# Optimization experiments

Measured on AMD Instinct MI355X. Metric: run time of the kernel, lower is better.

Reference implementation:

```python
import jax, jax.numpy as jnp
import numpy as np

D_MODEL = 1024
N_HEADS = 16
HEAD_DIM = D_MODEL // N_HEADS
D_FF = 4 * D_MODEL
EPS = 1e-5


def _layer_norm(h, g, b):
    m = jnp.mean(h, axis=-1, keepdims=True)
    v = jnp.mean(jnp.square(h - m), axis=-1, keepdims=True)
    return (h - m) * jax.lax.rsqrt(v + EPS) * g + b


def setup_inputs() -> dict:
    key = jax.random.key(0)
    ks = jax.random.split(key, 10)
    B, S, D = 4, 2048, D_MODEL
    scale = 0.02
    inp = {
        "x": jax.random.normal(ks[0], (B, S, D), dtype=jnp.float32),
        "Wq": scale * jax.random.normal(ks[1], (D, D), dtype=jnp.float32),
        "Wk": scale * jax.random.normal(ks[2], (D, D), dtype=jnp.float32),
        "Wv": scale * jax.random.normal(ks[3], (D, D), dtype=jnp.float32),
        "Wo": scale * jax.random.normal(ks[4], (D, D), dtype=jnp.float32),
        "ln1_g": jnp.ones((D,), dtype=jnp.float32),
        "ln1_b": jnp.zeros((D,), dtype=jnp.float32),
        "ln2_g": jnp.ones((D,), dtype=jnp.float32),
        "ln2_b": jnp.zeros((D,), dtype=jnp.float32),
        "W1": scale * jax.random.normal(ks[5], (D, D_FF), dtype=jnp.float32),
        "b1": jnp.zeros((D_FF,), dtype=jnp.float32),
        "W2": scale * jax.random.normal(ks[6], (D_FF, D), dtype=jnp.float32),
        "b2": jnp.zeros((D,), dtype=jnp.float32),
        "Wc": scale * jax.random.normal(ks[7], (D, 1), dtype=jnp.float32),
        "bc": jnp.zeros((1,), dtype=jnp.float32),
    }
    return inp


def reference(x, Wq, Wk, Wv, Wo, ln1_g, ln1_b, ln2_g, ln2_b, W1, b1, W2, b2, Wc, bc):
    B, S, D = x.shape
    H, hd = N_HEADS, HEAD_DIM
    # --- causal self-attention (pre-LN) ---
    h = _layer_norm(x, ln1_g, ln1_b)
    q = (h @ Wq).reshape(B, S, H, hd).transpose(0, 2, 1, 3)  # [B,H,S,hd]
    k = (h @ Wk).reshape(B, S, H, hd).transpose(0, 2, 1, 3)
    v = (h @ Wv).reshape(B, S, H, hd).transpose(0, 2, 1, 3)
    scores = jnp.einsum("bhqd,bhkd->bhqk", q, k) / jnp.sqrt(jnp.asarray(hd, x.dtype))
    causal = jnp.triu(jnp.ones((S, S), dtype=bool), k=1)
    scores = jnp.where(causal[None, None, :, :], -jnp.inf, scores)
    attn = jax.nn.softmax(scores, axis=-1)
    ctx = jnp.einsum("bhqk,bhkd->bhqd", attn, v).transpose(0, 2, 1, 3).reshape(B, S, D)
    x1 = x + ctx @ Wo
    # --- FFN (pre-LN, ReLU) ---
    h2 = _layer_norm(x1, ln2_g, ln2_b)
    ff = jax.nn.relu(h2 @ W1 + b1) @ W2 + b2
    x_out = x1 + ff
    # --- adaptive confidence gate: mean-pool seq -> Linear -> sigmoid -> batch mean ---
    pooled = jnp.mean(x_out, axis=1)  # [B,D]
    conf = jnp.mean(jax.nn.sigmoid(pooled @ Wc + bc), axis=0)  # [1]
    return x_out, conf
```

## Files before the change

kernel.cpp:

```cpp
#include <hip/hip_runtime.h>
#include <hip/hip_bf16.h>

typedef __hip_bfloat16 bf16;
typedef __attribute__((ext_vector_type(8))) short short8;
typedef __attribute__((ext_vector_type(4))) float f32x4;

#define D_MODELC 1024
#define D_FFC    4096
#define NHEADS   16
#define HDIM     64
#define SEQLEN   2048
#define BATCHN   4
#define MTOT     (BATCHN * SEQLEN)

__device__ __forceinline__ void async16(void* lds, const void* g) {
  __builtin_amdgcn_global_load_lds(
      (const __attribute__((address_space(1))) unsigned int*)g,
      (__attribute__((address_space(3))) unsigned int*)lds, 16, 0, 0);
}

__global__ __launch_bounds__(256) void transpose_bf16_k(
    const float* __restrict__ src, bf16* __restrict__ dst, int R, int C, float scale) {
  __shared__ float tile[32][33];
  int tx = threadIdx.x & 31, ty = threadIdx.x >> 5;
  int r0 = blockIdx.y * 32, c0 = blockIdx.x * 32;
#pragma unroll
  for (int i = 0; i < 4; i++) {
    int r = ty + i * 8;
    tile[r][tx] = src[(size_t)(r0 + r) * C + c0 + tx];
  }
  __syncthreads();
#pragma unroll
  for (int i = 0; i < 4; i++) {
    int c = ty + i * 8;
    dst[(size_t)(c0 + c) * R + r0 + tx] = __float2bfloat16(tile[tx][c] * scale);
  }
}

__global__ __launch_bounds__(256) void ln_bf16_k(
    const float* __restrict__ x, const float* __restrict__ g,
    const float* __restrict__ b, bf16* __restrict__ out) {
  int row = blockIdx.x;
  int t = threadIdx.x;
  f32x4 v = ((const f32x4*)(x + (size_t)row * D_MODELC))[t];
  float s = v[0] + v[1] + v[2] + v[3];
  float ss = v[0] * v[0] + v[1] * v[1] + v[2] * v[2] + v[3] * v[3];
#pragma unroll
  for (int m = 1; m < 64; m <<= 1) {
    s += __shfl_xor(s, m);
    ss += __shfl_xor(ss, m);
  }
  __shared__ float red[8];
  int w = t >> 6, l = t & 63;
  if (l == 0) { red[w] = s; red[4 + w] = ss; }
  __syncthreads();
  s = red[0] + red[1] + red[2] + red[3];
  ss = red[4] + red[5] + red[6] + red[7];
  float mean = s * (1.0f / D_MODELC);
  float var = ss * (1.0f / D_MODELC) - mean * mean;
  float rs = rsqrtf(var + 1e-5f);
  f32x4 gv = ((const f32x4*)g)[t];
  f32x4 bv = ((const f32x4*)b)[t];
  unsigned short u[4];
#pragma unroll
  for (int j = 0; j < 4; j++) {
    float o = (v[j] - mean) * rs * gv[j] + bv[j];
    u[j] = __bfloat16_as_ushort(__float2bfloat16(o));
  }
  unsigned int lo = (unsigned int)u[0] | ((unsigned int)u[1] << 16);
  unsigned int hi = (unsigned int)u[2] | ((unsigned int)u[3] << 16);
  ((uint2*)(out + (size_t)row * D_MODELC))[t] = make_uint2(lo, hi);
}

#define BM 128
#define BN 128
#define BKK 64

enum { EPI_QKV = 0, EPI_RESID = 1, EPI_BIAS_RELU = 2, EPI_BIAS_RESID = 3 };

template <int EPI>
__global__ __launch_bounds__(256) void gemm_nt(
    const bf16* __restrict__ A, const bf16* __restrict__ BT, int M, int N, int K,
    const float* __restrict__ bias, const float* __restrict__ resid,
    float* __restrict__ outF, bf16* __restrict__ outB) {
  __shared__ bf16 As[BM * BKK];
  __shared__ bf16 Bs[BN * BKK];
  const int t = threadIdx.x;
  const int l = t & 63;
  const int w = t >> 6;
  const int wm = w >> 1, wn = w & 1;

  int nwg = gridDim.x * gridDim.y;
  int bid = blockIdx.y * gridDim.x + blockIdx.x;
  if ((nwg & 7) == 0) {
    int q8 = nwg >> 3;
    bid = (bid & 7) * q8 + (bid >> 3);
  }
  const int bx = bid % gridDim.x, by = bid / gridDim.x;
  const int m0 = by * BM, n0 = bx * BN;
  const int lr = l & 15, lkg = l >> 4;

  f32x4 acc[4][4];
#pragma unroll
  for (int i = 0; i < 4; i++)
#pragma unroll
    for (int j = 0; j < 4; j++) acc[i][j] = (f32x4){0.f, 0.f, 0.f, 0.f};

  const char* Abase = (const char*)(A + (size_t)m0 * K);
  const char* Bbase = (const char*)(BT + (size_t)n0 * K);

  for (int k0 = 0; k0 < K; k0 += BKK) {
#pragma unroll
    for (int c = 0; c < 4; c++) {
      int off = (c * 256 + t) * 16;
      int r = off >> 7;
      int sg = ((off >> 4) & 7) ^ (r & 7);
      async16((char*)As + off, Abase + ((size_t)r * K + k0) * 2 + sg * 16);
      async16((char*)Bs + off, Bbase + ((size_t)r * K + k0) * 2 + sg * 16);
    }
    __syncthreads();
    short8 a[2][4], b[2][4];
#pragma unroll
    for (int kk = 0; kk < 2; kk++) {
#pragma unroll
      for (int mi = 0; mi < 4; mi++) {
        int row = wm * 64 + mi * 16 + lr;
        int sl = (kk * 4 + lkg) ^ (row & 7);
        a[kk][mi] = *(const short8*)((const char*)As + row * 128 + sl * 16);
      }
#pragma unroll
      for (int ni = 0; ni < 4; ni++) {
        int row = wn * 64 + ni * 16 + lr;
        int sl = (kk * 4 + lkg) ^ (row & 7);
        b[kk][ni] = *(const short8*)((const char*)Bs + row * 128 + sl * 16);
      }
    }
#pragma unroll
    for (int kk = 0; kk < 2; kk++)
#pragma unroll
      for (int mi = 0; mi < 4; mi++)
#pragma unroll
        for (int ni = 0; ni < 4; ni++)
          acc[mi][ni] = __builtin_amdgcn_mfma_f32_16x16x32_bf16(a[kk][mi], b[kk][ni], acc[mi][ni], 0, 0, 0);
    __syncthreads();
  }

#pragma unroll
  for (int mi = 0; mi < 4; mi++) {
#pragma unroll
    for (int ni = 0; ni < 4; ni++) {
#pragma unroll
      for (int j = 0; j < 4; j++) {
        int gm = m0 + wm * 64 + mi * 16 + ((l >> 4) * 4) + j;
        int gn = n0 + wn * 64 + ni * 16 + lr;
        float v = acc[mi][ni][j];
        if constexpr (EPI == EPI_QKV) {
          int sel = gn >> 10, d = gn & 1023;
          int b_ = gm >> 11, s_ = gm & 2047;
          int h2 = d >> 6, dd = d & 63;
          size_t bh = (size_t)b_ * NHEADS + h2;
          size_t dst;
          if (sel < 2) {
            dst = (size_t)sel * ((size_t)MTOT * D_MODELC) +
                  (bh * SEQLEN + s_) * HDIM + dd;
          } else {
            dst = 2 * ((size_t)MTOT * D_MODELC) +
                  (bh * HDIM + dd) * SEQLEN + s_;
          }
          outB[dst] = __float2bfloat16(v);
        } else if constexpr (EPI == EPI_RESID) {
          size_t idx = (size_t)gm * N + gn;
          outF[idx] = resid[idx] + v;
        } else if constexpr (EPI == EPI_BIAS_RELU) {
          float z = v + bias[gn];
          outB[(size_t)gm * N + gn] = __float2bfloat16(z > 0.f ? z : 0.f);
        } else {
          size_t idx = (size_t)gm * N + gn;
          outF[idx] = resid[idx] + v + bias[gn];
        }
      }
    }
  }
}

#define KVB 64
#define QB2 128
#define PSTR 76

__global__ __launch_bounds__(256) void attn_k(
    const bf16* __restrict__ qg, const bf16* __restrict__ kg,
    const bf16* __restrict__ vtg, bf16* __restrict__ ctx) {
  const int bid = blockIdx.x;
  const int qt = (SEQLEN / QB2 - 1) - (bid >> 6);
  const int bh = bid & 63;
  const int q0 = qt * QB2;
  const int t = threadIdx.x, w = t >> 6, l = t & 63;
  const int lr = l & 15, lkg = l >> 4, lk = lkg * 8;

  const bf16* Q  = qg  + (size_t)bh * SEQLEN * HDIM;
  const bf16* Kg = kg  + (size_t)bh * SEQLEN * HDIM;
  const bf16* Vt = vtg + (size_t)bh * HDIM * SEQLEN;

  __shared__ bf16 Ks[KVB * PSTR];
  __shared__ bf16 Vs[HDIM * PSTR];
  __shared__ bf16 Ps[4][32 * PSTR];

  short8 qf[2][2];
#pragma unroll
  for (int mi = 0; mi < 2; mi++)
#pragma unroll
    for (int kk = 0; kk < 2; kk++)
      qf[mi][kk] = *(const short8*)&Q[(size_t)(q0 + w * 32 + mi * 16 + lr) * HDIM + kk * 32 + lk];

  const short8 bones = {0x3F80, 0x3F80, 0x3F80, 0x3F80, 0x3F80, 0x3F80, 0x3F80, 0x3F80};

  f32x4 o[2][4];
  f32x4 ol[2];
#pragma unroll
  for (int mi = 0; mi < 2; mi++) {
    ol[mi] = (f32x4){0.f, 0.f, 0.f, 0.f};
#pragma unroll
    for (int nh = 0; nh < 4; nh++) o[mi][nh] = (f32x4){0.f, 0.f, 0.f, 0.f};
  }

  const int srow = t >> 3;
  const int scc  = (t & 7) * 8;

  const int ntiles = 2 * qt + 2;
  for (int tkv = 0; tkv < ntiles; tkv++) {
    const int kv0 = tkv * KVB;
#pragma unroll
    for (int r = 0; r < 2; r++) {
      int row = srow + r * 32;
      short8 kv = *(const short8*)&Kg[(size_t)(kv0 + row) * HDIM + scc];
      *(short8*)&Ks[row * PSTR + scc] = kv;
      short8 vv = *(const short8*)&Vt[(size_t)row * SEQLEN + kv0 + scc];
      *(short8*)&Vs[row * PSTR + scc] = vv;
    }
    __syncthreads();

    const bool active = (kv0 <= q0 + w * 32 + 31);
    if (active) {
      short8 kf[4][2];
#pragma unroll
      for (int ni = 0; ni < 4; ni++)
#pragma unroll
        for (int kk = 0; kk < 2; kk++)
          kf[ni][kk] = *(const short8*)&Ks[(ni * 16 + lr) * PSTR + kk * 32 + lk];
      f32x4 s[2][4];
#pragma unroll
      for (int mi = 0; mi < 2; mi++)
#pragma unroll
        for (int ni = 0; ni < 4; ni++) {
          f32x4 a = (f32x4){0.f, 0.f, 0.f, 0.f};
#pragma unroll
          for (int kk = 0; kk < 2; kk++)
            a = __builtin_amdgcn_mfma_f32_16x16x32_bf16(qf[mi][kk], kf[ni][kk], a, 0, 0, 0);
          s[mi][ni] = a;
        }
      if (tkv >= ntiles - 2) {
#pragma unroll
        for (int mi = 0; mi < 2; mi++)
#pragma unroll
          for (int ni = 0; ni < 4; ni++)
#pragma unroll
            for (int j = 0; j < 4; j++) {
              int qq = q0 + w * 32 + mi * 16 + lkg * 4 + j;
              int kv = kv0 + ni * 16 + lr;
              if (kv > qq) s[mi][ni][j] = -1e30f;
            }
      }
#pragma unroll
      for (int mi = 0; mi < 2; mi++)
#pragma unroll
        for (int ni = 0; ni < 4; ni++)
#pragma unroll
          for (int j = 0; j < 4; j++)
            ((short*)Ps[w])[(mi * 16 + lkg * 4 + j) * PSTR + ni * 16 + lr] =
                (short)__bfloat16_as_ushort(__float2bfloat16(exp2f(s[mi][ni][j])));
#pragma unroll
      for (int kk = 0; kk < 2; kk++) {
        short8 pa[2];
#pragma unroll
        for (int mi = 0; mi < 2; mi++) {
          pa[mi] = *(const short8*)&Ps[w][(mi * 16 + lr) * PSTR + kk * 32 + lk];
          ol[mi] = __builtin_amdgcn_mfma_f32_16x16x32_bf16(pa[mi], bones, ol[mi], 0, 0, 0);
        }
#pragma unroll
        for (int nh = 0; nh < 4; nh++) {
          short8 vb = *(const short8*)&Vs[(nh * 16 + lr) * PSTR + kk * 32 + lk];
#pragma unroll
          for (int mi = 0; mi < 2; mi++)
            o[mi][nh] = __builtin_amdgcn_mfma_f32_16x16x32_bf16(pa[mi], vb, o[mi][nh], 0, 0, 0);
        }
      }
    }
    __syncthreads();
  }

  const int b_ = bh >> 4, h_ = bh & 15;
#pragma unroll
  for (int mi = 0; mi < 2; mi++)
#pragma unroll
    for (int j = 0; j < 4; j++) {
      float inv = 1.0f / ol[mi][j];
      int qq = q0 + w * 32 + mi * 16 + lkg * 4 + j;
      size_t base = (((size_t)b_ * SEQLEN + qq) * NHEADS + h_) * HDIM;
#pragma unroll
      for (int nh = 0; nh < 4; nh++)
        ctx[base + nh * 16 + lr] = __float2bfloat16(o[mi][nh][j] * inv);
    }
}

__global__ __launch_bounds__(256) void pool_partial_k(
    const float* __restrict__ xo, float* __restrict__ part) {
  int blk = blockIdx.x;
  int b_ = blk >> 4, ch = blk & 15;
  int t = threadIdx.x;
  f32x4 acc = (f32x4){0.f, 0.f, 0.f, 0.f};
  const float* base = xo + ((size_t)b_ * SEQLEN + (size_t)ch * 128) * D_MODELC;
  for (int r = 0; r < 128; r++)
    acc += ((const f32x4*)(base + (size_t)r * D_MODELC))[t];
  ((f32x4*)(part + (size_t)blk * D_MODELC))[t] = acc;
}

__global__ __launch_bounds__(256) void conf_k(
    const float* __restrict__ part, const float* __restrict__ Wc,
    const float* __restrict__ bc, float* __restrict__ outc) {
  int t = threadIdx.x;
  __shared__ float red[4];
  float total = 0.f;
  for (int b_ = 0; b_ < BATCHN; b_++) {
    f32x4 sum = (f32x4){0.f, 0.f, 0.f, 0.f};
    for (int ch = 0; ch < 16; ch++)
      sum += ((const f32x4*)(part + (size_t)(b_ * 16 + ch) * D_MODELC))[t];
    f32x4 wv = ((const f32x4*)Wc)[t];
    float d = (sum[0] * wv[0] + sum[1] * wv[1] + sum[2] * wv[2] + sum[3] * wv[3]) * (1.0f / SEQLEN);
#pragma unroll
    for (int m = 1; m < 64; m <<= 1) d += __shfl_xor(d, m);
    int wq = t >> 6, l = t & 63;
    if (l == 0) red[wq] = d;
    __syncthreads();
    float z = red[0] + red[1] + red[2] + red[3] + bc[0];
    total += 1.0f / (1.0f + __expf(-z));
    __syncthreads();
  }
  if (t == 0) outc[0] = total * (1.0f / BATCHN);
}

extern "C" void kernel_launch(void* const* d_in, const int* in_sizes, int n_in,
                              void* d_out, int out_size, void* d_ws, size_t ws_size,
                              hipStream_t stream) {
  const float* x    = (const float*)d_in[0];
  const float* Wq   = (const float*)d_in[1];
  const float* Wk   = (const float*)d_in[2];
  const float* Wv   = (const float*)d_in[3];
  const float* Wo   = (const float*)d_in[4];
  const float* ln1g = (const float*)d_in[5];
  const float* ln1b = (const float*)d_in[6];
  const float* ln2g = (const float*)d_in[7];
  const float* ln2b = (const float*)d_in[8];
  const float* W1   = (const float*)d_in[9];
  const float* b1   = (const float*)d_in[10];
  const float* W2   = (const float*)d_in[11];
  const float* b2   = (const float*)d_in[12];
  const float* Wc   = (const float*)d_in[13];
  const float* bc   = (const float*)d_in[14];

  char* ws = (char*)d_ws;
  const size_t MB = 1024 * 1024;
  bf16* qkv   = (bf16*)(ws);
  bf16* ctx   = (bf16*)(ws + 48 * MB);
  bf16* ff1   = (bf16*)(ws);
  bf16* h     = (bf16*)(ws + 64 * MB);
  bf16* WqkvT = (bf16*)(ws + 80 * MB);
  bf16* WoT   = (bf16*)(ws + 86 * MB);
  bf16* W1T   = (bf16*)(ws + 88 * MB);
  bf16* W2T   = (bf16*)(ws + 96 * MB);
  float* part = (float*)(ws + 104 * MB);

  float* xout = (float*)d_out;
  dim3 blk(256);

  const float SCL2 = 0.125f * 1.44269504f;

  transpose_bf16_k<<<dim3(32, 32), blk, 0, stream>>>(Wq, WqkvT, 1024, 1024, SCL2);
  transpose_bf16_k<<<dim3(32, 32), blk, 0, stream>>>(Wk, WqkvT + 1024 * 1024, 1024, 1024, 1.0f);
  transpose_bf16_k<<<dim3(32, 32), blk, 0, stream>>>(Wv, WqkvT + 2 * 1024 * 1024, 1024, 1024, 1.0f);
  transpose_bf16_k<<<dim3(32, 32), blk, 0, stream>>>(Wo, WoT, 1024, 1024, 1.0f);
  transpose_bf16_k<<<dim3(128, 32), blk, 0, stream>>>(W1, W1T, 1024, 4096, 1.0f);
  transpose_bf16_k<<<dim3(32, 128), blk, 0, stream>>>(W2, W2T, 4096, 1024, 1.0f);

  ln_bf16_k<<<MTOT, blk, 0, stream>>>(x, ln1g, ln1b, h);
  gemm_nt<EPI_QKV><<<dim3(3072 / BN, MTOT / BM), blk, 0, stream>>>(
      h, WqkvT, MTOT, 3072, 1024, nullptr, nullptr, nullptr, qkv);
  attn_k<<<dim3((SEQLEN / QB2) * 64), blk, 0, stream>>>(
      qkv, qkv + (size_t)MTOT * D_MODELC, qkv + 2 * (size_t)MTOT * D_MODELC, ctx);
  gemm_nt<EPI_RESID><<<dim3(1024 / BN, MTOT / BM), blk, 0, stream>>>(
      ctx, WoT, MTOT, 1024, 1024, nullptr, x, xout, nullptr);
  ln_bf16_k<<<MTOT, blk, 0, stream>>>(xout, ln2g, ln2b, h);
  gemm_nt<EPI_BIAS_RELU><<<dim3(4096 / BN, MTOT / BM), blk, 0, stream>>>(
      h, W1T, MTOT, 4096, 1024, b1, nullptr, nullptr, ff1);
  gemm_nt<EPI_BIAS_RESID><<<dim3(1024 / BN, MTOT / BM), blk, 0, stream>>>(
      ff1, W2T, MTOT, 1024, 4096, b2, xout, xout, nullptr);
  pool_partial_k<<<64, blk, 0, stream>>>(xout, part);
  conf_k<<<1, blk, 0, stream>>>(part, Wc, bc, xout + (size_t)MTOT * D_MODELC);
}
```

Measured before the change: 414.3 us.

## Add 256x256 double-buffered 8-wave GEMM for QKV and FFN1 projections

Adds a new GEMM kernel with 256x256 tiles, 512 threads and double-buffered LDS. Asynchronous global-to-LDS loads are interleaved with four MFMA phases per k-step, using explicit waitcnt, barriers and setprio. The QKV and first FFN projections now use it, which raises data reuse per tile and overlaps memory traffic with compute. The epilogue is moved into a shared helper. The LDS footprint is large (128KB), the tile-to-block mapping hardcodes M=8192, and the hand-scheduled waits must be exactly right to stay correct.

```diff
diff --git a/kernel.cpp b/kernel.cpp
--- a/kernel.cpp
+++ b/kernel.cpp
@@ -72,11 +72,40 @@
   ((uint2*)(out + (size_t)row * D_MODELC))[t] = make_uint2(lo, hi);
 }
 
+enum { EPI_QKV = 0, EPI_RESID = 1, EPI_BIAS_RELU = 2, EPI_BIAS_RESID = 3 };
+
+template <int EPI>
+__device__ __forceinline__ void epi_write(
+    int gm, int gn, float v, int N,
+    const float* __restrict__ bias, const float* __restrict__ resid,
+    float* __restrict__ outF, bf16* __restrict__ outB) {
+  if constexpr (EPI == EPI_QKV) {
+    int sel = gn >> 10, d = gn & 1023;
+    int b_ = gm >> 11, s_ = gm & 2047;
+    int h2 = d >> 6, dd = d & 63;
+    size_t bh = (size_t)b_ * NHEADS + h2;
+    size_t dst;
+    if (sel < 2) {
+      dst = (size_t)sel * ((size_t)MTOT * D_MODELC) + (bh * SEQLEN + s_) * HDIM + dd;
+    } else {
+      dst = 2 * ((size_t)MTOT * D_MODELC) + (bh * HDIM + dd) * SEQLEN + s_;
+    }
+    outB[dst] = __float2bfloat16(v);
+  } else if constexpr (EPI == EPI_RESID) {
+    size_t idx = (size_t)gm * N + gn;
+    outF[idx] = resid[idx] + v;
+  } else if constexpr (EPI == EPI_BIAS_RELU) {
+    float z = v + bias[gn];
+    outB[(size_t)gm * N + gn] = __float2bfloat16(z > 0.f ? z : 0.f);
+  } else {
+    size_t idx = (size_t)gm * N + gn;
+    outF[idx] = resid[idx] + v + bias[gn];
+  }
+}
+
 #define BM 128
 #define BN 128
 #define BKK 64
-
-enum { EPI_QKV = 0, EPI_RESID = 1, EPI_BIAS_RELU = 2, EPI_BIAS_RESID = 3 };
 
 template <int EPI>
 __global__ __launch_bounds__(256) void gemm_nt(
@@ -146,40 +175,180 @@
   }
 
 #pragma unroll
-  for (int mi = 0; mi < 4; mi++) {
+  for (int mi = 0; mi < 4; mi++)
+#pragma unroll
+    for (int ni = 0; ni < 4; ni++)
+#pragma unroll
+      for (int j = 0; j < 4; j++) {
+        int gm = m0 + wm * 64 + mi * 16 + lkg * 4 + j;
+        int gn = n0 + wn * 64 + ni * 16 + lr;
+        epi_write<EPI>(gm, gn, acc[mi][ni][j], N, bias, resid, outF, outB);
+      }
+}
+
+#define GBM 256
+#define GBN 256
+#define GBK 64
+
+template <int EPI>
+__global__ __launch_bounds__(512, 2) void gemm8p(
+    const bf16* __restrict__ A, const bf16* __restrict__ BT, int N, int K,
+    const float* __restrict__ bias, const float* __restrict__ resid,
+    float* __restrict__ outF, bf16* __restrict__ outB) {
+  __shared__ bf16 As[2][GBM * GBK];
+  __shared__ bf16 Bs[2][GBN * GBK];
+  const int t = threadIdx.x;
+  const int l = t & 63, wid = t >> 6;
+  const int wr = wid >> 2, wc = wid & 3;
+  const int lr = l & 15, lkg = l >> 4;
+
+  int nwg = gridDim.x;
+  int bid = blockIdx.x;
+  int sb = (bid & 7) * (nwg >> 3) + (bid >> 3);
+  const int by = sb & 31;
+  const int bx = sb >> 5;
+  const int m0 = by * GBM, n0 = bx * GBN;
+
+  const char* Abase = (const char*)(A + (size_t)m0 * K);
+  const char* Bbase = (const char*)(BT + (size_t)n0 * K);
+  const int NT = K >> 6;
+
+  f32x4 acc[8][4];
+#pragma unroll
+  for (int i = 0; i < 8; i++)
+#pragma unroll
+    for (int j = 0; j < 4; j++) acc[i][j] = (f32x4){0.f, 0.f, 0.f, 0.f};
+
+  int aoff[2][2][4], boff[2][4];
+#pragma unroll
+  for (int H = 0; H < 2; H++)
+#pragma unroll
+    for (int kk = 0; kk < 2; kk++)
+#pragma unroll
+      for (int mi = 0; mi < 4; mi++) {
+        int row = wr * 128 + H * 64 + mi * 16 + lr;
+        aoff[H][kk][mi] = row * 128 + (((kk * 4 + lkg) ^ (row & 7)) * 16);
+      }
+#pragma unroll
+  for (int kk = 0; kk < 2; kk++)
 #pragma unroll
     for (int ni = 0; ni < 4; ni++) {
+      int row = wc * 64 + ni * 16 + lr;
+      boff[kk][ni] = row * 128 + (((kk * 4 + lkg) ^ (row & 7)) * 16);
+    }
+
+#define STG(ldsArr, gbase, buf, half, k0)                                        \
+  {                                                                              \
+    _Pragma("unroll")                                                            \
+    for (int ld = 0; ld < 2; ld++) {                                             \
+      int off = (ld * 512 + t) * 16;                                             \
+      int r = (off >> 7) + (half) * 128;                                         \
+      int sg = ((off >> 4) & 7) ^ (r & 7);                                       \
+      async16((char*)ldsArr[buf] + (half) * 16384 + off,                         \
+              gbase + ((size_t)r * K + (k0)) * 2 + sg * 16);                     \
+    }                                                                            \
+  }
+
+  STG(Bs, Bbase, 0, 0, 0);
+  STG(Bs, Bbase, 0, 1, 0);
+  STG(As, Abase, 0, 0, 0);
+  STG(As, Abase, 0, 1, 0);
+  {
+    int k1 = (NT > 1) ? GBK : 0;
+    STG(Bs, Bbase, 1, 0, k1);
+    STG(Bs, Bbase, 1, 1, k1);
+    STG(As, Abase, 1, 0, k1);
+  }
+  asm volatile("s_waitcnt vmcnt(6)" ::: "memory");
+  __builtin_amdgcn_s_barrier();
+
+  for (int kt = 0; kt < NT; kt++) {
+    const int cb = kt & 1;
+    const char* Ab = (const char*)As[cb];
+    const char* Bb = (const char*)Bs[cb];
+    const int kA1 = (kt + 1 < NT) ? (kt + 1) * GBK : 0;
+    const int kN  = (kt + 2 < NT) ? (kt + 2) * GBK : 0;
+    short8 b[4][2], a[4];
+
+#pragma unroll
+    for (int ni = 0; ni < 4; ni++) {
+      b[ni][0] = *(const short8*)(Bb + boff[0][ni]);
+      b[ni][1] = *(const short8*)(Bb + boff[1][ni]);
+    }
+#pragma unroll
+    for (int mi = 0; mi < 4; mi++) a[mi] = *(const short8*)(Ab + aoff[0][0][mi]);
+    STG(As, Abase, cb ^ 1, 1, kA1);
+    __builtin_amdgcn_s_barrier();
+    asm volatile("s_waitcnt lgkmcnt(0)" ::: "memory");
+    __builtin_amdgcn_sched_barrier(0);
+    __builtin_amdgcn_s_setprio(1);
+#pragma unroll
+    for (int mi = 0; mi < 4; mi++)
+#pragma unroll
+      for (int ni = 0; ni < 4; ni++)
+        acc[mi][ni] = __builtin_amdgcn_mfma_f32_16x16x32_bf16(a[mi], b[ni][0], acc[mi][ni], 0, 0, 0);
+    __builtin_amdgcn_s_setprio(0);
+    __builtin_amdgcn_s_barrier();
+
+#pragma unroll
+    for (int mi = 0; mi < 4; mi++) a[mi] = *(const short8*)(Ab + aoff[0][1][mi]);
+    STG(Bs, Bbase, cb, 0, kN);
+    __builtin_amdgcn_s_barrier();
+    asm volatile("s_waitcnt lgkmcnt(0)" ::: "memory");
+    __builtin_amdgcn_sched_barrier(0);
+    __builtin_amdgcn_s_setprio(1);
+#pragma unroll
+    for (int mi = 0; mi < 4; mi++)
+#pragma unroll
+      for (int ni = 0; ni < 4; ni++)
+        acc[mi][ni] = __builtin_amdgcn_mfma_f32_16x16x32_bf16(a[mi], b[ni][1], acc[mi][ni], 0, 0, 0);
+    __builtin_amdgcn_s_setprio(0);
+    __builtin_amdgcn_s_barrier();
+
+#pragma unroll
+    for (int mi = 0; mi < 4; mi++) a[mi] = *(const short8*)(Ab + aoff[1][0][mi]);
+    STG(Bs, Bbase, cb, 1, kN);
+    __builtin_amdgcn_s_barrier();
+    asm volatile("s_waitcnt lgkmcnt(0)" ::: "memory");
+    __builtin_amdgcn_sched_barrier(0);
+    __builtin_amdgcn_s_setprio(1);
+#pragma unroll
+    for (int mi = 0; mi < 4; mi++)
+#pragma unroll
+      for (int ni = 0; ni < 4; ni++)
+        acc[4 + mi][ni] = __builtin_amdgcn_mfma_f32_16x16x32_bf16(a[mi], b[ni][0], acc[4 + mi][ni], 0, 0, 0);
+    __builtin_amdgcn_s_setprio(0);
+    __builtin_amdgcn_s_barrier();
+
+#pragma unroll
+    for (int mi = 0; mi < 4; mi++) a[mi] = *(const short8*)(Ab + aoff[1][1][mi]);
+    STG(As, Abase, cb, 0, kN);
+    asm volatile("s_waitcnt vmcnt(6)" ::: "memory");
+    __builtin_amdgcn_s_barrier();
+    asm volatile("s_waitcnt lgkmcnt(0)" ::: "memory");
+    __builtin_amdgcn_sched_barrier(0);
+    __builtin_amdgcn_s_setprio(1);
+#pragma unroll
+    for (int mi = 0; mi < 4; mi++)
+#pragma unroll
+      for (int ni = 0; ni < 4; ni++)
+        acc[4 + mi][ni] = __builtin_amdgcn_mfma_f32_16x16x32_bf16(a[mi], b[ni][1], acc[4 + mi][ni], 0, 0, 0);
+    __builtin_amdgcn_s_setprio(0);
+    __builtin_amdgcn_s_barrier();
+  }
+#undef STG
+
+#pragma unroll
+  for (int I = 0; I < 8; I++) {
+    int rowoff = (I >> 2) * 64 + (I & 3) * 16;
+#pragma unroll
+    for (int ni = 0; ni < 4; ni++)
 #pragma unroll
       for (int j = 0; j < 4; j++) {
-        int gm = m0 + wm * 64 + mi * 16 + ((l >> 4) * 4) + j;
-        int gn = n0 + wn * 64 + ni * 16 + lr;
-        float v = acc[mi][ni][j];
-        if constexpr (EPI == EPI_QKV) {
-          int sel = gn >> 10, d = gn & 1023;
-          int b_ = gm >> 11, s_ = gm & 2047;
-          int h2 = d >> 6, dd = d & 63;
-          size_t bh = (size_t)b_ * NHEADS + h2;
-          size_t dst;
-          if (sel < 2) {
-            dst = (size_t)sel * ((size_t)MTOT * D_MODELC) +
-                  (bh * SEQLEN + s_) * HDIM + dd;
-          } else {
-            dst = 2 * ((size_t)MTOT * D_MODELC) +
-                  (bh * HDIM + dd) * SEQLEN + s_;
-          }
-          outB[dst] = __float2bfloat16(v);
-        } else if constexpr (EPI == EPI_RESID) {
-          size_t idx = (size_t)gm * N + gn;
-          outF[idx] = resid[idx] + v;
-        } else if constexpr (EPI == EPI_BIAS_RELU) {
-          float z = v + bias[gn];
-          outB[(size_t)gm * N + gn] = __float2bfloat16(z > 0.f ? z : 0.f);
-        } else {
-          size_t idx = (size_t)gm * N + gn;
-          outF[idx] = resid[idx] + v + bias[gn];
-        }
-      }
-    }
+        int gm = m0 + wr * 128 + rowoff + lkg * 4 + j;
+        int gn = n0 + wc * 64 + ni * 16 + lr;
+        epi_write<EPI>(gm, gn, acc[I][ni][j], N, bias, resid, outF, outB);
+      }
   }
 }
 
@@ -381,6 +550,7 @@
 
   float* xout = (float*)d_out;
   dim3 blk(256);
+  dim3 blk512(512);
 
   const float SCL2 = 0.125f * 1.44269504f;
 
@@ -392,15 +562,15 @@
   transpose_bf16_k<<<dim3(32, 128), blk, 0, stream>>>(W2, W2T, 4096, 1024, 1.0f);
 
   ln_bf16_k<<<MTOT, blk, 0, stream>>>(x, ln1g, ln1b, h);
-  gemm_nt<EPI_QKV><<<dim3(3072 / BN, MTOT / BM), blk, 0, stream>>>(
-      h, WqkvT, MTOT, 3072, 1024, nullptr, nullptr, nullptr, qkv);
+  gemm8p<EPI_QKV><<<dim3((3072 / GBN) * 32), blk512, 0, stream>>>(
+      h, WqkvT, 3072, 1024, nullptr, nullptr, nullptr, qkv);
   attn_k<<<dim3((SEQLEN / QB2) * 64), blk, 0, stream>>>(
       qkv, qkv + (size_t)MTOT * D_MODELC, qkv + 2 * (size_t)MTOT * D_MODELC, ctx);
   gemm_nt<EPI_RESID><<<dim3(1024 / BN, MTOT / BM), blk, 0, stream>>>(
       ctx, WoT, MTOT, 1024, 1024, nullptr, x, xout, nullptr);
   ln_bf16_k<<<MTOT, blk, 0, stream>>>(xout, ln2g, ln2b, h);
-  gemm_nt<EPI_BIAS_RELU><<<dim3(4096 / BN, MTOT / BM), blk, 0, stream>>>(
-      h, W1T, MTOT, 4096, 1024, b1, nullptr, nullptr, ff1);
+  gemm8p<EPI_BIAS_RELU><<<dim3((4096 / GBN) * 32), blk512, 0, stream>>>(
+      h, W1T, 4096, 1024, b1, nullptr, nullptr, ff1);
   gemm_nt<EPI_BIAS_RESID><<<dim3(1024 / BN, MTOT / BM), blk, 0, stream>>>(
       ff1, W2T, MTOT, 1024, 4096, b2, xout, xout, nullptr);
   pool_partial_k<<<64, blk, 0, stream>>>(xout, part);
```

After: 443.1 us. 6.9% more time.
